# Optimization experiments

Hardware: AMD Instinct MI355X
Metric: run time of the kernel (lower is better)

Reference implementation:

```python
import jax, jax.numpy as jnp
import numpy as np

# Dims: P patterns, L pattern length, D word dim, V vocab, H mlp hidden, C classes, N doc length
P, L, D, V, H, C, N = 256, 6, 300, 100000, 256, 5, 4096


def setup_inputs() -> dict:
    key = jax.random.key(0)
    ks = jax.random.split(key, 10)
    doc = jax.random.randint(ks[0], (N,), 0, V)
    emb = jax.random.normal(ks[1], (V, D), dtype=jnp.float32)
    diags = jax.random.normal(ks[2], (P * 2 * L, D), dtype=jnp.float32)
    diags = diags / jnp.linalg.norm(diags, axis=1, keepdims=True)  # normalize() at init
    bias = jax.random.normal(ks[3], (P * 2 * L, 1), dtype=jnp.float32)
    epsilon = jax.random.normal(ks[4], (P, L - 1), dtype=jnp.float32)
    w0 = jax.random.normal(ks[5], (H, P), dtype=jnp.float32) * 0.05
    b0 = jnp.zeros((H,), jnp.float32)
    w1 = jax.random.normal(ks[6], (H, H), dtype=jnp.float32) * 0.05
    b1 = jnp.zeros((H,), jnp.float32)
    w2 = jax.random.normal(ks[7], (C, H), dtype=jnp.float32) * 0.05
    b2 = jnp.zeros((C,), jnp.float32)
    return dict(doc=doc, emb=emb, diags=diags, bias=bias, epsilon=epsilon,
                w0=w0, b0=b0, w1=w1, b1=b1, w2=w2, b2=b2)


def reference(doc, emb, diags, bias, epsilon, w0, b0, w1, b1, w2, b2):
    # fixed scalar gates: epsilon_scale = self_loop_scale = 0.5 (non-trainable)
    sls = jax.nn.sigmoid(jnp.float32(0.5))
    eps_val = jax.nn.sigmoid(jnp.float32(0.5)) * jax.nn.sigmoid(epsilon)  # [P, L-1]

    # precompute all per-token transition matrices in one GEMM
    x = emb[doc]                                                # [N, D]
    T = jax.nn.sigmoid(x @ diags.T + bias[:, 0])                # [N, P*2*L]
    T = T.reshape(-1, P, 2, L)                                  # [N, P, 2, L]

    h0 = jnp.zeros((P, L), jnp.float32).at[:, 0].set(1.0)
    zero_pad = jnp.zeros((P, 1), jnp.float32)
    one_pad = jnp.ones((P, 1), jnp.float32)

    def step(h, Tt):  # transition_once, fused over tokens via scan
        main = jnp.concatenate([zero_pad, h[:, :-1] * Tt[:, 1, :-1]], axis=1) \
               + sls * h * Tt[:, 0, :]
        h2 = main + jnp.concatenate([one_pad, main[:, :-1] * eps_val], axis=1)
        return h2, h2[:, -1]

    _, last_states = jax.lax.scan(step, h0, T)                  # last_states: [N, P]
    scores = last_states.sum(axis=0)                            # [P]

    # MLP (num_mlp_layers=2 hidden ReLU layers, then linear to classes)
    z = scores[None, :]                                         # [1, P]
    z = jax.nn.relu(z @ w0.T + b0)
    z = jax.nn.relu(z @ w1.T + b1)
    return z @ w2.T + b2                                        # [1, C]
```

## Files before the change

kernel.cpp:

```cpp
#include <hip/hip_runtime.h>
#include <hip/hip_bf16.h>
#include <cstdint>
#include <cstddef>

#define P_ 256
#define L_ 6
#define D_ 300
#define J_ 3072
#define N_ 4096
#define H_ 256
#define C_ 5
#define KP 320
#define KSTEPS 10

#define SLS 0.62245933120185459f

typedef __attribute__((ext_vector_type(8))) short short8v;
typedef __attribute__((ext_vector_type(4))) short short4v;
typedef __attribute__((ext_vector_type(4))) float f32x4;

__device__ __forceinline__ float sigmoidf_(float x) { return 1.0f / (1.0f + __expf(-x)); }
__device__ __forceinline__ float bf2f(short s) { return __uint_as_float(((unsigned)(unsigned short)s) << 16); }

__global__ __launch_bounds__(256) void prep_XB(
    const int* __restrict__ doc, const float* __restrict__ emb,
    const float* __restrict__ diags,
    __hip_bfloat16* __restrict__ X, __hip_bfloat16* __restrict__ Bb,
    int* __restrict__ cnt)
{
    const int i = blockIdx.x * 256 + threadIdx.x;
    if (i == 0) cnt[0] = 0;
    const int NX = N_ * KP;
    if (i < NX) {
        const int n = i / KP, k = i - n * KP;
        float v = (k < D_) ? emb[(size_t)doc[n] * D_ + k] : 0.0f;
        X[i] = __float2bfloat16(v);
    } else {
        const int ii = i - NX;
        const int j = ii / KP, k = ii - j * KP;
        float v = (k < D_) ? diags[(size_t)j * D_ + k] : 0.0f;
        Bb[ii] = __float2bfloat16(v);
    }
}

__global__ __launch_bounds__(256) void gemm_mfma(
    const __hip_bfloat16* __restrict__ X, const __hip_bfloat16* __restrict__ Bb,
    const float* __restrict__ bias, __hip_bfloat16* __restrict__ Tt)
{
    __shared__ __hip_bfloat16 As[2][128 * 32];
    __shared__ __hip_bfloat16 Bs[2][128 * 32];

    const int tid  = threadIdx.x;
    const int lane = tid & 63;
    const int w    = tid >> 6;
    const int wr   = w >> 1, wc = w & 1;

    const int bid = blockIdx.x;
    const int swz = (bid & 7) * 96 + (bid >> 3);
    const int bx  = swz % 24, by = swz / 24;
    const int m0  = by * 128;
    const int j0  = bx * 128;

    const int srow = w * 32 + (lane >> 2);
    const int scol = (lane & 3) * 8;

    f32x4 acc[4][4];
    #pragma unroll
    for (int m = 0; m < 4; ++m)
        #pragma unroll
        for (int n = 0; n < 4; ++n)
            acc[m][n] = (f32x4){0.f, 0.f, 0.f, 0.f};

    const int fr = lane & 15;
    const int kg = (lane >> 4) * 8;

    auto stage = [&](int kt, int b) {
        const int k0 = kt * 32;
        #pragma unroll
        for (int q = 0; q < 2; ++q) {
            const __hip_bfloat16* ga = X + (size_t)(m0 + srow + q * 16) * KP + k0 + scol;
            __builtin_amdgcn_global_load_lds(
                (const __attribute__((address_space(1))) unsigned*)ga,
                (__attribute__((address_space(3))) unsigned*)(&As[b][(w * 2 + q) * 512]),
                16, 0, 0);
            const __hip_bfloat16* gb = Bb + (size_t)(j0 + srow + q * 16) * KP + k0 + scol;
            __builtin_amdgcn_global_load_lds(
                (const __attribute__((address_space(1))) unsigned*)gb,
                (__attribute__((address_space(3))) unsigned*)(&Bs[b][(w * 2 + q) * 512]),
                16, 0, 0);
        }
    };

    stage(0, 0);
    __syncthreads();

    int buf = 0;
    for (int kt = 0; kt < KSTEPS; ++kt) {
        if (kt + 1 < KSTEPS) stage(kt + 1, buf ^ 1);

        short8v a[4], b[4];
        #pragma unroll
        for (int m = 0; m < 4; ++m)
            a[m] = *(const short8v*)(&As[buf][(wr * 64 + m * 16 + fr) * 32 + kg]);
        #pragma unroll
        for (int n = 0; n < 4; ++n)
            b[n] = *(const short8v*)(&Bs[buf][(wc * 64 + n * 16 + fr) * 32 + kg]);
        #pragma unroll
        for (int m = 0; m < 4; ++m)
            #pragma unroll
            for (int n = 0; n < 4; ++n)
                acc[m][n] = __builtin_amdgcn_mfma_f32_16x16x32_bf16(a[m], b[n], acc[m][n], 0, 0, 0);

        __syncthreads();
        buf ^= 1;
    }

    #pragma unroll
    for (int n = 0; n < 4; ++n) {
        const int j = j0 + wc * 64 + n * 16 + fr;
        const float bj = bias[j];
        #pragma unroll
        for (int m = 0; m < 4; ++m) {
            const int rbase = m0 + wr * 64 + m * 16 + (lane >> 4) * 4;
            short4v pk;
            #pragma unroll
            for (int r = 0; r < 4; ++r) {
                float v = acc[m][n][r] + bj;
                __hip_bfloat16 hb = __float2bfloat16(sigmoidf_(v));
                pk[r] = *reinterpret_cast<const short*>(&hb);
            }
            *(short4v*)(Tt + (size_t)j * N_ + rbase) = pk;
        }
    }
}

__device__ __forceinline__ void compose_maps(const float* C, const float* R, float* N)
{
    #pragma unroll
    for (int j = 0; j < 7; ++j) {
        #pragma unroll
        for (int i = 0; i < 6; ++i) {
            float a = (j == 6) ? C[42 + i] : 0.0f;
            #pragma unroll
            for (int u = 0; u < 6; ++u) a = fmaf(C[u * 7 + i], R[j * 7 + u], a);
            N[j * 7 + i] = a;
        }
        float sa = R[j * 7 + 6] + ((j == 6) ? C[48] : 0.0f);
        #pragma unroll
        for (int u = 0; u < 6; ++u) sa = fmaf(C[u * 7 + 6], R[j * 7 + u], sa);
        N[j * 7 + 6] = sa;
    }
}

__global__ __launch_bounds__(256) void scan_tree_mlp(
    const __hip_bfloat16* __restrict__ Tt, const float* __restrict__ epsilon,
    float* __restrict__ scores, int* __restrict__ cnt,
    const float* __restrict__ w0, const float* __restrict__ b0,
    const float* __restrict__ w1, const float* __restrict__ b1,
    const float* __restrict__ w2, const float* __restrict__ b2,
    float* __restrict__ out)
{
    __shared__ float lds[256 * 49];
    __shared__ int lastBlk;
    const int tid = threadIdx.x;
    const int p   = blockIdx.x;

    {
        const int c = tid;
        float ep[5];
        #pragma unroll
        for (int l = 0; l < 5; ++l)
            ep[l] = SLS * (1.0f / (1.0f + __expf(-epsilon[p * 5 + l])));

        float hc[7][6], sc[7];
        #pragma unroll
        for (int j = 0; j < 7; ++j) {
            sc[j] = 0.0f;
            #pragma unroll
            for (int i = 0; i < 6; ++i) hc[j][i] = (i == j) ? 1.0f : 0.0f;
        }

        #pragma unroll
        for (int h = 0; h < 2; ++h) {
            short8v v[12];
            #pragma unroll
            for (int l = 0; l < 12; ++l)
                v[l] = *(const short8v*)(Tt + (size_t)(p * 12 + l) * N_ + c * 16 + h * 8);

            #pragma unroll
            for (int tt = 0; tt < 8; ++tt) {
                float sT0[6], T1v[6];
                #pragma unroll
                for (int l = 0; l < 6; ++l) {
                    sT0[l] = SLS * bf2f(v[l][tt]);
                    T1v[l] = bf2f(v[6 + l][tt]);
                }
                #pragma unroll
                for (int j = 0; j < 7; ++j) {
                    float m[6];
                    m[0] = hc[j][0] * sT0[0];
                    #pragma unroll
                    for (int i = 1; i < 6; ++i)
                        m[i] = fmaf(hc[j][i - 1], T1v[i - 1], hc[j][i] * sT0[i]);
                    hc[j][0] = m[0] + ((j == 6) ? 1.0f : 0.0f);
                    #pragma unroll
                    for (int i = 1; i < 6; ++i)
                        hc[j][i] = fmaf(m[i - 1], ep[i - 1], m[i]);
                    sc[j] += hc[j][5];
                }
            }
        }

        #pragma unroll
        for (int j = 0; j < 7; ++j) {
            #pragma unroll
            for (int i = 0; i < 6; ++i) lds[c * 49 + j * 7 + i] = hc[j][i];
            lds[c * 49 + j * 7 + 6] = sc[j];
        }
    }

    for (int act = 128; act >= 1; act >>= 1) {
        __syncthreads();
        float Nn[49];
        const bool on = (tid < act);
        if (on) compose_maps(&lds[(2 * tid + 1) * 49], &lds[(2 * tid) * 49], Nn);
        __syncthreads();
        if (on) {
            #pragma unroll
            for (int q = 0; q < 49; ++q) lds[tid * 49 + q] = Nn[q];
        }
    }

    if (tid == 0) {
        scores[p] = lds[6] + lds[48];
        __threadfence();
        int ret = __hip_atomic_fetch_add(cnt, 1, __ATOMIC_ACQ_REL,
                                         __HIP_MEMORY_SCOPE_AGENT);
        lastBlk = (ret == P_ - 1);
    }
    __syncthreads();
    if (!lastBlk) return;

    __threadfence();
    __syncthreads();

    {
        float* s0 = lds;
        float* z0 = lds + 256;
        float* z1 = lds + 512;

        s0[tid] = scores[tid];
        __syncthreads();

        float acc = b0[tid];
        {
            const float4* wr = (const float4*)(w0 + (size_t)tid * P_);
            #pragma unroll 4
            for (int q = 0; q < P_ / 4; ++q) {
                float4 w = wr[q];
                acc = fmaf(w.x, s0[q * 4 + 0], acc);
                acc = fmaf(w.y, s0[q * 4 + 1], acc);
                acc = fmaf(w.z, s0[q * 4 + 2], acc);
                acc = fmaf(w.w, s0[q * 4 + 3], acc);
            }
        }
        z0[tid] = fmaxf(acc, 0.0f);
        __syncthreads();

        acc = b1[tid];
        {
            const float4* wr = (const float4*)(w1 + (size_t)tid * H_);
            #pragma unroll 4
            for (int q = 0; q < H_ / 4; ++q) {
                float4 w = wr[q];
                acc = fmaf(w.x, z0[q * 4 + 0], acc);
                acc = fmaf(w.y, z0[q * 4 + 1], acc);
                acc = fmaf(w.z, z0[q * 4 + 2], acc);
                acc = fmaf(w.w, z0[q * 4 + 3], acc);
            }
        }
        z1[tid] = fmaxf(acc, 0.0f);
        __syncthreads();

        if (tid < C_) {
            float o = b2[tid];
            const float* wr = w2 + (size_t)tid * H_;
            for (int hh = 0; hh < H_; ++hh) o = fmaf(wr[hh], z1[hh], o);
            out[tid] = o;
        }
    }
}

extern "C" void kernel_launch(void* const* d_in, const int* in_sizes, int n_in,
                              void* d_out, int out_size, void* d_ws, size_t ws_size,
                              hipStream_t stream)
{
    const int*   doc     = (const int*)d_in[0];
    const float* emb     = (const float*)d_in[1];
    const float* diags   = (const float*)d_in[2];
    const float* bias    = (const float*)d_in[3];
    const float* epsilon = (const float*)d_in[4];
    const float* w0      = (const float*)d_in[5];
    const float* b0      = (const float*)d_in[6];
    const float* w1      = (const float*)d_in[7];
    const float* b1      = (const float*)d_in[8];
    const float* w2      = (const float*)d_in[9];
    const float* b2      = (const float*)d_in[10];
    float* out = (float*)d_out;

    float* scores = (float*)d_ws;
    int*   cnt    = (int*)(scores + P_);
    __hip_bfloat16* Tt = (__hip_bfloat16*)((float*)d_ws + 512);
    __hip_bfloat16* X  = Tt + (size_t)J_ * N_;
    __hip_bfloat16* Bb = X  + (size_t)N_ * KP;

    prep_XB<<<(N_ * KP + J_ * KP) / 256, 256, 0, stream>>>(doc, emb, diags, X, Bb, cnt);
    gemm_mfma<<<(J_ / 128) * (N_ / 128), 256, 0, stream>>>(X, Bb, bias, Tt);
    scan_tree_mlp<<<P_, 256, 0, stream>>>(Tt, epsilon, scores, cnt,
                                          w0, b0, w1, b1, w2, b2, out);
}
```

Measured before the change: 72.51 us.

## Vectorize prep, add dedicated MLP block that prefetches weights and spins on flags

The prep kernel now reads and converts four floats per thread with float4 loads, launching a quarter of the threads. The scan kernel gains an extra block that touches all MLP weights to warm the cache, then polls per-pattern padded flags set with release stores. This replaces the last-block atomic counter, so the MLP can start as soon as all scores are written and its weight loads overlap the scan. The spinning block relies on all 257 blocks being co-resident and adds polling traffic.

Measured after the change: 98.43 us. 1.36x slower.

```diff
diff --git a/kernel.cpp b/kernel.cpp
--- a/kernel.cpp
+++ b/kernel.cpp
@@ -21,25 +21,38 @@
 
 __device__ __forceinline__ float sigmoidf_(float x) { return 1.0f / (1.0f + __expf(-x)); }
 __device__ __forceinline__ float bf2f(short s) { return __uint_as_float(((unsigned)(unsigned short)s) << 16); }
+__device__ __forceinline__ short f2bf(float f) {
+    __hip_bfloat16 h = __float2bfloat16(f);
+    return *reinterpret_cast<const short*>(&h);
+}
+
+__device__ __forceinline__ int rmw_peek(int* p) {
+    return __hip_atomic_fetch_add(p, 0, __ATOMIC_RELAXED, __HIP_MEMORY_SCOPE_AGENT);
+}
 
 __global__ __launch_bounds__(256) void prep_XB(
     const int* __restrict__ doc, const float* __restrict__ emb,
     const float* __restrict__ diags,
     __hip_bfloat16* __restrict__ X, __hip_bfloat16* __restrict__ Bb,
-    int* __restrict__ cnt)
+    int* __restrict__ flags)
 {
     const int i = blockIdx.x * 256 + threadIdx.x;
-    if (i == 0) cnt[0] = 0;
-    const int NX = N_ * KP;
-    if (i < NX) {
-        const int n = i / KP, k = i - n * KP;
-        float v = (k < D_) ? emb[(size_t)doc[n] * D_ + k] : 0.0f;
-        X[i] = __float2bfloat16(v);
+    if (i < P_ * 16) flags[i] = 0;
+    const int NX4 = N_ * (KP / 4);
+    float4 v = {0.f, 0.f, 0.f, 0.f};
+    if (i < NX4) {
+        const int n = i / (KP / 4), k4 = i - n * (KP / 4);
+        if (k4 < D_ / 4)
+            v = ((const float4*)(emb + (size_t)doc[n] * D_))[k4];
+        short4v pk = { f2bf(v.x), f2bf(v.y), f2bf(v.z), f2bf(v.w) };
+        *(short4v*)(X + (size_t)i * 4) = pk;
     } else {
-        const int ii = i - NX;
-        const int j = ii / KP, k = ii - j * KP;
-        float v = (k < D_) ? diags[(size_t)j * D_ + k] : 0.0f;
-        Bb[ii] = __float2bfloat16(v);
+        const int ii = i - NX4;
+        const int j = ii / (KP / 4), k4 = ii - j * (KP / 4);
+        if (k4 < D_ / 4)
+            v = ((const float4*)(diags + (size_t)j * D_))[k4];
+        short4v pk = { f2bf(v.x), f2bf(v.y), f2bf(v.z), f2bf(v.w) };
+        *(short4v*)(Bb + (size_t)ii * 4) = pk;
     }
 }
 
@@ -124,11 +137,8 @@
             const int rbase = m0 + wr * 64 + m * 16 + (lane >> 4) * 4;
             short4v pk;
             #pragma unroll
-            for (int r = 0; r < 4; ++r) {
-                float v = acc[m][n][r] + bj;
-                __hip_bfloat16 hb = __float2bfloat16(sigmoidf_(v));
-                pk[r] = *reinterpret_cast<const short*>(&hb);
-            }
+            for (int r = 0; r < 4; ++r)
+                pk[r] = f2bf(sigmoidf_(acc[m][n][r] + bj));
             *(short4v*)(Tt + (size_t)j * N_ + rbase) = pk;
         }
     }
@@ -152,96 +162,111 @@
     }
 }
 
-__global__ __launch_bounds__(256) void scan_tree_mlp(
+__global__ __launch_bounds__(256) void scan_mlp(
     const __hip_bfloat16* __restrict__ Tt, const float* __restrict__ epsilon,
-    float* __restrict__ scores, int* __restrict__ cnt,
+    float* __restrict__ scores, int* __restrict__ flags,
     const float* __restrict__ w0, const float* __restrict__ b0,
     const float* __restrict__ w1, const float* __restrict__ b1,
     const float* __restrict__ w2, const float* __restrict__ b2,
     float* __restrict__ out)
 {
     __shared__ float lds[256 * 49];
-    __shared__ int lastBlk;
     const int tid = threadIdx.x;
-    const int p   = blockIdx.x;
+    const int bid = blockIdx.x;
+
+    if (bid < P_) {
+        const int p = bid;
+        {
+            const int c = tid;
+            float ep[5];
+            #pragma unroll
+            for (int l = 0; l < 5; ++l)
+                ep[l] = SLS * (1.0f / (1.0f + __expf(-epsilon[p * 5 + l])));
+
+            float hc[7][6], sc[7];
+            #pragma unroll
+            for (int j = 0; j < 7; ++j) {
+                sc[j] = 0.0f;
+                #pragma unroll
+                for (int i = 0; i < 6; ++i) hc[j][i] = (i == j) ? 1.0f : 0.0f;
+            }
+
+            #pragma unroll
+            for (int h = 0; h < 2; ++h) {
+                short8v v[12];
+                #pragma unroll
+                for (int l = 0; l < 12; ++l)
+                    v[l] = *(const short8v*)(Tt + (size_t)(p * 12 + l) * N_ + c * 16 + h * 8);
+
+                #pragma unroll
+                for (int tt = 0; tt < 8; ++tt) {
+                    float sT0[6], T1v[6];
+                    #pragma unroll
+                    for (int l = 0; l < 6; ++l) {
+                        sT0[l] = SLS * bf2f(v[l][tt]);
+                        T1v[l] = bf2f(v[6 + l][tt]);
+                    }
+                    #pragma unroll
+                    for (int j = 0; j < 7; ++j) {
+                        float m[6];
+                        m[0] = hc[j][0] * sT0[0];
+                        #pragma unroll
+                        for (int i = 1; i < 6; ++i)
+                            m[i] = fmaf(hc[j][i - 1], T1v[i - 1], hc[j][i] * sT0[i]);
+                        hc[j][0] = m[0] + ((j == 6) ? 1.0f : 0.0f);
+                        #pragma unroll
+                        for (int i = 1; i < 6; ++i)
+                            hc[j][i] = fmaf(m[i - 1], ep[i - 1], m[i]);
+                        sc[j] += hc[j][5];
+                    }
+                }
+            }
+
+            #pragma unroll
+            for (int j = 0; j < 7; ++j) {
+                #pragma unroll
+                for (int i = 0; i < 6; ++i) lds[c * 49 + j * 7 + i] = hc[j][i];
+                lds[c * 49 + j * 7 + 6] = sc[j];
+            }
+        }
+
+        for (int act = 128; act >= 1; act >>= 1) {
+            __syncthreads();
+            float Nn[49];
+            const bool on = (tid < act);
+            if (on) compose_maps(&lds[(2 * tid + 1) * 49], &lds[(2 * tid) * 49], Nn);
+            __syncthreads();
+            if (on) {
+                #pragma unroll
+                for (int q = 0; q < 49; ++q) lds[tid * 49 + q] = Nn[q];
+            }
+        }
+
+        if (tid == 0) {
+            scores[p] = lds[6] + lds[48];
+            __threadfence();
+            __hip_atomic_store(&flags[p * 16], 1, __ATOMIC_RELEASE,
+                               __HIP_MEMORY_SCOPE_AGENT);
+        }
+        return;
+    }
 
     {
-        const int c = tid;
-        float ep[5];
-        #pragma unroll
-        for (int l = 0; l < 5; ++l)
-            ep[l] = SLS * (1.0f / (1.0f + __expf(-epsilon[p * 5 + l])));
-
-        float hc[7][6], sc[7];
-        #pragma unroll
-        for (int j = 0; j < 7; ++j) {
-            sc[j] = 0.0f;
-            #pragma unroll
-            for (int i = 0; i < 6; ++i) hc[j][i] = (i == j) ? 1.0f : 0.0f;
-        }
-
-        #pragma unroll
-        for (int h = 0; h < 2; ++h) {
-            short8v v[12];
-            #pragma unroll
-            for (int l = 0; l < 12; ++l)
-                v[l] = *(const short8v*)(Tt + (size_t)(p * 12 + l) * N_ + c * 16 + h * 8);
-
-            #pragma unroll
-            for (int tt = 0; tt < 8; ++tt) {
-                float sT0[6], T1v[6];
-                #pragma unroll
-                for (int l = 0; l < 6; ++l) {
-                    sT0[l] = SLS * bf2f(v[l][tt]);
-                    T1v[l] = bf2f(v[6 + l][tt]);
-                }
-                #pragma unroll
-                for (int j = 0; j < 7; ++j) {
-                    float m[6];
-                    m[0] = hc[j][0] * sT0[0];
-                    #pragma unroll
-                    for (int i = 1; i < 6; ++i)
-                        m[i] = fmaf(hc[j][i - 1], T1v[i - 1], hc[j][i] * sT0[i]);
-                    hc[j][0] = m[0] + ((j == 6) ? 1.0f : 0.0f);
-                    #pragma unroll
-                    for (int i = 1; i < 6; ++i)
-                        hc[j][i] = fmaf(m[i - 1], ep[i - 1], m[i]);
-                    sc[j] += hc[j][5];
-                }
-            }
-        }
-
-        #pragma unroll
-        for (int j = 0; j < 7; ++j) {
-            #pragma unroll
-            for (int i = 0; i < 6; ++i) lds[c * 49 + j * 7 + i] = hc[j][i];
-            lds[c * 49 + j * 7 + 6] = sc[j];
-        }
-    }
-
-    for (int act = 128; act >= 1; act >>= 1) {
-        __syncthreads();
-        float Nn[49];
-        const bool on = (tid < act);
-        if (on) compose_maps(&lds[(2 * tid + 1) * 49], &lds[(2 * tid) * 49], Nn);
-        __syncthreads();
-        if (on) {
-            #pragma unroll
-            for (int q = 0; q < 49; ++q) lds[tid * 49 + q] = Nn[q];
-        }
-    }
-
-    if (tid == 0) {
-        scores[p] = lds[6] + lds[48];
-        __threadfence();
-        int ret = __hip_atomic_fetch_add(cnt, 1, __ATOMIC_ACQ_REL,
-                                         __HIP_MEMORY_SCOPE_AGENT);
-        lastBlk = (ret == P_ - 1);
+        float acc = 0.f;
+        for (int idx = tid; idx < (H_ * P_) / 4; idx += 256)
+            { float4 v = ((const float4*)w0)[idx]; acc += v.x + v.y + v.z + v.w; }
+        for (int idx = tid; idx < (H_ * H_) / 4; idx += 256)
+            { float4 v = ((const float4*)w1)[idx]; acc += v.x + v.y + v.z + v.w; }
+        for (int idx = tid; idx < (C_ * H_) / 4; idx += 256)
+            { float4 v = ((const float4*)w2)[idx]; acc += v.x + v.y + v.z + v.w; }
+        asm volatile("" :: "v"(acc));
+    }
+
+    {
+        while (rmw_peek(&flags[tid * 16]) == 0) __builtin_amdgcn_s_sleep(4);
     }
     __syncthreads();
-    if (!lastBlk) return;
-
-    __threadfence();
+    if (tid == 0) __threadfence();
     __syncthreads();
 
     {
@@ -309,13 +334,13 @@
     float* out = (float*)d_out;
 
     float* scores = (float*)d_ws;
-    int*   cnt    = (int*)(scores + P_);
-    __hip_bfloat16* Tt = (__hip_bfloat16*)((float*)d_ws + 512);
+    int*   flags  = (int*)(scores + P_);
+    __hip_bfloat16* Tt = (__hip_bfloat16*)((int*)flags + P_ * 16);
     __hip_bfloat16* X  = Tt + (size_t)J_ * N_;
     __hip_bfloat16* Bb = X  + (size_t)N_ * KP;
 
-    prep_XB<<<(N_ * KP + J_ * KP) / 256, 256, 0, stream>>>(doc, emb, diags, X, Bb, cnt);
+    prep_XB<<<(N_ * KP + J_ * KP) / 1024, 256, 0, stream>>>(doc, emb, diags, X, Bb, flags);
     gemm_mfma<<<(J_ / 128) * (N_ / 128), 256, 0, stream>>>(X, Bb, bias, Tt);
-    scan_tree_mlp<<<P_, 256, 0, stream>>>(Tt, epsilon, scores, cnt,
-                                          w0, b0, w1, b1, w2, b2, out);
-}
+    scan_mlp<<<P_ + 1, 256, 0, stream>>>(Tt, epsilon, scores, flags,
+                                         w0, b0, w1, b1, w2, b2, out);
+}
```
